# Optimization experiments

Hardware: AMD Instinct MI355X
Metric: run time of the kernel (lower is better)

The kernel has to match this reference:

```python
import jax, jax.numpy as jnp
import numpy as np


def _eta(pos, conj):
    # e[0] = pos[:,1::2] repeated into even/odd cols; e[1] = (+/-)pos[:,0::2] likewise
    c = jnp.repeat(pos[:, 1::2], 2, axis=1)
    s = jnp.repeat(pos[:, 0::2], 2, axis=1)
    return jnp.stack([c, s if conj else -s])  # [2, N, d]


def setup_inputs() -> dict:
    key = jax.random.key(0)
    ks = jax.random.split(key, 8)
    B, N, d, H = 8, 4096, 128, 4
    s = 0.02
    return {
        "x": jax.random.normal(ks[0], (B, N, d), jnp.float32),
        "pos": jax.random.normal(ks[1], (N, d), jnp.float32),
        "W_lt": jax.random.normal(ks[2], (d, d), jnp.float32) * s,
        "W_phi": jax.random.normal(ks[3], (d * H, d), jnp.float32) * s,
        "b_phi": jnp.zeros((d * H,), jnp.float32),
        "W_c1": jax.random.normal(ks[4], (H, H), jnp.float32) * s,
        "b_c1": jnp.zeros((H,), jnp.float32),
        "W_c2": jax.random.normal(ks[5], (1, H), jnp.float32) * s,
        "b_c2": jnp.zeros((1,), jnp.float32),
        "ln_g": jnp.ones((d,), jnp.float32),
        "ln_b": jnp.zeros((d,), jnp.float32),
        "W_f1": jax.random.normal(ks[6], (d, d), jnp.float32) * s,
        "b_f1": jnp.zeros((d,), jnp.float32),
        "W_f2": jax.random.normal(ks[7], (d, d), jnp.float32) * s,
        "b_f2": jnp.zeros((d,), jnp.float32),
    }


def reference(x, pos, W_lt, W_phi, b_phi, W_c1, b_c1, W_c2, b_c2,
              ln_g, ln_b, W_f1, b_f1, W_f2, b_f2):
    B, N, d = x.shape
    H = W_phi.shape[0] // d
    x = x @ W_lt.T                                   # linear_trans (no bias)
    e = _eta(pos, False)                             # [2,N,d]
    xe = x[None] * e[:, None]                        # [2,B,N,d]
    # A = ones(N,N) - I  =>  A @ v == sum over nodes minus self
    f = xe.sum(axis=2, keepdims=True) - xe           # [2,B,N,d]
    f_norm = jnp.sqrt(f[0] ** 2 + f[1] ** 2)         # [B,N,d]
    phi = ((x + pos[None]) @ W_phi.T + b_phi).reshape(B, N, H, d)
    # ReLU1(|f| - phi): relu(min(1, f_norm - phi))
    res = jax.nn.relu(jnp.minimum(1.0, f_norm[:, :, None, :] - phi))  # [B,N,H,d]
    ce = _eta(pos, True)
    fec = f[0] * ce[0][None] - f[1] * ce[1][None]    # [B,N,d]
    rfe = res * fec[:, :, None, :]                   # [B,N,H,d]
    # inverse transform: (1/N) * (M @ A) with A symmetric => sum-minus-self over node dim
    inv = (rfe.sum(axis=1, keepdims=True) - rfe) / N  # [B,N,H,d]
    t = inv.transpose(0, 1, 3, 2)                    # [B,N,d,H]
    comb = (jax.nn.relu(t @ W_c1.T + b_c1) @ W_c2.T + b_c2)[..., 0]  # [B,N,d]
    m = x + comb
    mu = m.mean(-1, keepdims=True)
    var = ((m - mu) ** 2).mean(-1, keepdims=True)
    mn = (m - mu) * jax.lax.rsqrt(var + 1e-6) * ln_g + ln_b
    return jax.nn.relu(mn @ W_f1.T + b_f1) @ W_f2.T + b_f2
```

## Files before the change

kernel.cpp:

```cpp
#include <hip/hip_runtime.h>
#include <hip/hip_bf16.h>


#define DEV __device__ __forceinline__

typedef __attribute__((ext_vector_type(8))) short bf16x8;
typedef __attribute__((ext_vector_type(4))) float f32x4;

constexpr int Bb = 8, Nn = 4096;
constexpr int BN = Bb * Nn;
constexpr int LDP = 136;

union U8 { ushort u[8]; uint4 v; };

static DEV ushort f2bf(float f) {
    __hip_bfloat16 h = __float2bfloat16(f);
    return *reinterpret_cast<unsigned short*>(&h);
}
static DEV float bf2f(ushort u) {
    return __bfloat162float(*reinterpret_cast<const __hip_bfloat16*>(&u));
}

template <int MODE>
__global__ __launch_bounds__(256) void k_mfma_gemm(
    const void* __restrict__ Xv, const float* __restrict__ W,
    const float* __restrict__ bias, const float* __restrict__ pos,
    ushort* __restrict__ outB)
{
    __shared__ __align__(16) ushort xs[64 * LDP];
    __shared__ __align__(16) ushort wsl[128 * LDP];
    const int t = threadIdx.x;
    const int row0 = blockIdx.x * 64;
    const int jt = (MODE == 1) ? blockIdx.y : 0;

    if (MODE == 0) {
        const float* X = (const float*)Xv;
        #pragma unroll
        for (int i = 0; i < 4; ++i) {
            int e = t + i * 256, r = e >> 4, c = (e & 15) * 8;
            const float* p = X + (size_t)(row0 + r) * 128 + c;
            float4 a = *reinterpret_cast<const float4*>(p);
            float4 b = *reinterpret_cast<const float4*>(p + 4);
            U8 u;
            u.u[0] = f2bf(a.x); u.u[1] = f2bf(a.y); u.u[2] = f2bf(a.z); u.u[3] = f2bf(a.w);
            u.u[4] = f2bf(b.x); u.u[5] = f2bf(b.y); u.u[6] = f2bf(b.z); u.u[7] = f2bf(b.w);
            *reinterpret_cast<uint4*>(xs + r * LDP + c) = u.v;
        }
    } else {
        const ushort* X = (const ushort*)Xv;
        #pragma unroll
        for (int i = 0; i < 4; ++i) {
            int e = t + i * 256, r = e >> 4, c = (e & 15) * 8;
            U8 u;
            u.v = *reinterpret_cast<const uint4*>(X + (size_t)(row0 + r) * 128 + c);
            int n = (row0 + r) & (Nn - 1);
            const float* q = pos + (size_t)n * 128 + c;
            float4 pa = *reinterpret_cast<const float4*>(q);
            float4 pb = *reinterpret_cast<const float4*>(q + 4);
            u.u[0] = f2bf(bf2f(u.u[0]) + pa.x);
            u.u[1] = f2bf(bf2f(u.u[1]) + pa.y);
            u.u[2] = f2bf(bf2f(u.u[2]) + pa.z);
            u.u[3] = f2bf(bf2f(u.u[3]) + pa.w);
            u.u[4] = f2bf(bf2f(u.u[4]) + pb.x);
            u.u[5] = f2bf(bf2f(u.u[5]) + pb.y);
            u.u[6] = f2bf(bf2f(u.u[6]) + pb.z);
            u.u[7] = f2bf(bf2f(u.u[7]) + pb.w);
            *reinterpret_cast<uint4*>(xs + r * LDP + c) = u.v;
        }
    }
    {
        const float* Wt = W + (size_t)jt * 128 * 128;
        #pragma unroll
        for (int i = 0; i < 8; ++i) {
            int e = t + i * 256, r = e >> 4, c = (e & 15) * 8;
            const float* p = Wt + (size_t)r * 128 + c;
            float4 a = *reinterpret_cast<const float4*>(p);
            float4 b = *reinterpret_cast<const float4*>(p + 4);
            U8 u;
            u.u[0] = f2bf(a.x); u.u[1] = f2bf(a.y); u.u[2] = f2bf(a.z); u.u[3] = f2bf(a.w);
            u.u[4] = f2bf(b.x); u.u[5] = f2bf(b.y); u.u[6] = f2bf(b.z); u.u[7] = f2bf(b.w);
            *reinterpret_cast<uint4*>(wsl + r * LDP + c) = u.v;
        }
    }
    __syncthreads();

    const int w = t >> 6, l = t & 63;
    const int lr = l & 15;
    const int lk = (l >> 4) * 8;

    f32x4 acc[8];
    #pragma unroll
    for (int cf = 0; cf < 8; ++cf) acc[cf] = f32x4{0.f, 0.f, 0.f, 0.f};

    #pragma unroll
    for (int ks = 0; ks < 4; ++ks) {
        bf16x8 a = *reinterpret_cast<const bf16x8*>(xs + (w * 16 + lr) * LDP + ks * 32 + lk);
        #pragma unroll
        for (int cf = 0; cf < 8; ++cf) {
            bf16x8 b = *reinterpret_cast<const bf16x8*>(wsl + (cf * 16 + lr) * LDP + ks * 32 + lk);
            acc[cf] = __builtin_amdgcn_mfma_f32_16x16x32_bf16(a, b, acc[cf], 0, 0, 0);
        }
    }

    __syncthreads();

    #pragma unroll
    for (int cf = 0; cf < 8; ++cf) {
        int col = cf * 16 + lr;
        float bv = (MODE == 1) ? bias[jt * 128 + col] : 0.f;
        #pragma unroll
        for (int reg = 0; reg < 4; ++reg) {
            int rl = w * 16 + (l >> 4) * 4 + reg;
            xs[rl * LDP + col] = f2bf(acc[cf][reg] + bv);
        }
    }
    __syncthreads();

    #pragma unroll
    for (int i = 0; i < 4; ++i) {
        int e = t + i * 256, r = e >> 4, c = (e & 15) * 8;
        uint4 v = *reinterpret_cast<const uint4*>(xs + r * LDP + c);
        if (MODE == 0)
            *reinterpret_cast<uint4*>(outB + (size_t)(row0 + r) * 128 + c) = v;
        else
            *reinterpret_cast<uint4*>(outB + (size_t)(row0 + r) * 512 + jt * 128 + c) = v;
    }
}

__global__ __launch_bounds__(256) void k_reduceS(
    const ushort* __restrict__ x1b, const float* __restrict__ pos,
    float* __restrict__ PS)
{
    int b = blockIdx.x >> 6, c64 = blockIdx.x & 63;
    int rr = threadIdx.x >> 5, d0 = (threadIdx.x & 31) * 4;
    float a0[4] = {0,0,0,0}, a1[4] = {0,0,0,0};
    #pragma unroll
    for (int i = 0; i < 8; ++i) {
        int n = c64 * 64 + i * 8 + rr;
        size_t r = (size_t)b * Nn + n;
        ushort4 xv = *reinterpret_cast<const ushort4*>(x1b + r * 128 + d0);
        float4 p = *reinterpret_cast<const float4*>(pos + (size_t)n * 128 + d0);
        float x0 = bf2f(xv.x), x1 = bf2f(xv.y), x2 = bf2f(xv.z), x3 = bf2f(xv.w);
        a0[0] += x0 * p.y; a1[0] += x0 * p.x;
        a0[1] += x1 * p.y; a1[1] += x1 * p.x;
        a0[2] += x2 * p.w; a1[2] += x2 * p.z;
        a0[3] += x3 * p.w; a1[3] += x3 * p.z;
    }
    __shared__ float redA[8][128], redB[8][128];
    #pragma unroll
    for (int j = 0; j < 4; ++j) { redA[rr][d0 + j] = a0[j]; redB[rr][d0 + j] = a1[j]; }
    __syncthreads();
    int tt = threadIdx.x;
    float s = 0.f;
    if (tt < 128) {
        #pragma unroll
        for (int k = 0; k < 8; ++k) s += redA[k][tt];
    } else {
        #pragma unroll
        for (int k = 0; k < 8; ++k) s += redB[k][tt - 128];
    }
    PS[(size_t)blockIdx.x * 256 + tt] = s;
}

__global__ __launch_bounds__(256) void k_finS(
    const float* __restrict__ PS, float* __restrict__ S0, float* __restrict__ S1)
{
    int b = blockIdx.x, t = threadIdx.x;
    float s = 0.f;
    #pragma unroll 8
    for (int c = 0; c < 64; ++c) s += PS[(size_t)(b * 64 + c) * 256 + t];
    if (t < 128) S0[b * 128 + t] = s;
    else         S1[b * 128 + (t - 128)] = s;
}

__global__ __launch_bounds__(256) void k_reduceT(
    const ushort* __restrict__ x1b, const ushort* __restrict__ phi,
    const float* __restrict__ pos, const float* __restrict__ S0,
    const float* __restrict__ S1, float* __restrict__ PT)
{
    int b = blockIdx.x >> 6, c64 = blockIdx.x & 63;
    int rr = threadIdx.x >> 5, d0 = (threadIdx.x & 31) * 4;
    float4 S0v = *reinterpret_cast<const float4*>(S0 + b * 128 + d0);
    float4 S1v = *reinterpret_cast<const float4*>(S1 + b * 128 + d0);
    float acc[4][4];
    #pragma unroll
    for (int h = 0; h < 4; ++h)
        #pragma unroll
        for (int j = 0; j < 4; ++j) acc[h][j] = 0.f;

    #pragma unroll 2
    for (int i = 0; i < 8; ++i) {
        int n = c64 * 64 + i * 8 + rr;
        size_t r = (size_t)b * Nn + n;
        ushort4 xv4 = *reinterpret_cast<const ushort4*>(x1b + r * 128 + d0);
        float4 p = *reinterpret_cast<const float4*>(pos + (size_t)n * 128 + d0);
        float xv[4] = {bf2f(xv4.x), bf2f(xv4.y), bf2f(xv4.z), bf2f(xv4.w)};
        float cc[4] = {p.y, p.y, p.w, p.w};
        float ss[4] = {p.x, p.x, p.z, p.z};
        float fec[4], fn[4];
        #pragma unroll
        for (int j = 0; j < 4; ++j) {
            float f0 = ((j < 2) ? ((j == 0) ? S0v.x : S0v.y) : ((j == 2) ? S0v.z : S0v.w)) - xv[j] * cc[j];
            float f1 = xv[j] * ss[j] - ((j < 2) ? ((j == 0) ? S1v.x : S1v.y) : ((j == 2) ? S1v.z : S1v.w));
            fn[j] = sqrtf(f0 * f0 + f1 * f1);
            fec[j] = f0 * cc[j] - f1 * ss[j];
        }
        #pragma unroll
        for (int h = 0; h < 4; ++h) {
            ushort4 ph4 = *reinterpret_cast<const ushort4*>(phi + r * 512 + h * 128 + d0);
            float ph[4] = {bf2f(ph4.x), bf2f(ph4.y), bf2f(ph4.z), bf2f(ph4.w)};
            #pragma unroll
            for (int j = 0; j < 4; ++j)
                acc[h][j] += fmaxf(0.f, fminf(1.f, fn[j] - ph[j])) * fec[j];
        }
    }
    __shared__ float red[8][512];
    #pragma unroll
    for (int h = 0; h < 4; ++h)
        #pragma unroll
        for (int j = 0; j < 4; ++j) red[rr][h * 128 + d0 + j] = acc[h][j];
    __syncthreads();
    int tt = threadIdx.x;
    #pragma unroll
    for (int q = 0; q < 2; ++q) {
        int idx = tt + q * 256;
        float s = 0.f;
        #pragma unroll
        for (int k = 0; k < 8; ++k) s += red[k][idx];
        PT[(size_t)blockIdx.x * 512 + idx] = s;
    }
}

__global__ __launch_bounds__(256) void k_finT(
    const float* __restrict__ PT, float* __restrict__ T)
{
    int idx = blockIdx.x * 256 + threadIdx.x;
    int b = idx >> 9, lo = idx & 511;
    float s = 0.f;
    #pragma unroll 8
    for (int c = 0; c < 64; ++c) s += PT[(size_t)b * 32768 + c * 512 + lo];
    T[idx] = s;
}

__global__ __launch_bounds__(256) void k_comb_ln(
    const ushort* __restrict__ x1b, const ushort* __restrict__ phi,
    const float* __restrict__ pos, const float* __restrict__ S0,
    const float* __restrict__ S1, const float* __restrict__ T,
    const float* __restrict__ Wc1, const float* __restrict__ bc1,
    const float* __restrict__ Wc2, const float* __restrict__ bc2,
    const float* __restrict__ lng, const float* __restrict__ lnb,
    ushort* __restrict__ mnB)
{
    int w = threadIdx.x >> 6, l = threadIdx.x & 63;
    int rrow = blockIdx.x * 4 + w;
    int b = rrow >> 12;
    int n = rrow & 4095;
    int d0 = 2 * l;
    size_t r = (size_t)rrow;

    ushort2 xv2 = *reinterpret_cast<const ushort2*>(x1b + r * 128 + d0);
    float2 p2 = *reinterpret_cast<const float2*>(pos + (size_t)n * 128 + d0);
    float2 s0 = *reinterpret_cast<const float2*>(S0 + b * 128 + d0);
    float2 s1 = *reinterpret_cast<const float2*>(S1 + b * 128 + d0);
    float cc = p2.y, ss = p2.x;

    float m[2];
    float xv[2] = {bf2f(xv2.x), bf2f(xv2.y)};
    float S0a[2] = {s0.x, s0.y}, S1a[2] = {s1.x, s1.y};
    #pragma unroll
    for (int q = 0; q < 2; ++q) {
        float f0 = S0a[q] - xv[q] * cc;
        float f1 = xv[q] * ss - S1a[q];
        float fn = sqrtf(f0 * f0 + f1 * f1);
        float fec = f0 * cc - f1 * ss;
        float inv[4];
        #pragma unroll
        for (int h = 0; h < 4; ++h) {
            float ph = bf2f(phi[r * 512 + h * 128 + d0 + q]);
            float res = fmaxf(0.f, fminf(1.f, fn - ph));
            inv[h] = (T[(b * 4 + h) * 128 + d0 + q] - res * fec) * (1.f / (float)Nn);
        }
        float comb = bc2[0];
        #pragma unroll
        for (int h = 0; h < 4; ++h) {
            float u = bc1[h];
            #pragma unroll
            for (int h2 = 0; h2 < 4; ++h2) u += Wc1[h * 4 + h2] * inv[h2];
            comb += fmaxf(u, 0.f) * Wc2[h];
        }
        m[q] = xv[q] + comb;
    }

    float s = m[0] + m[1];
    #pragma unroll
    for (int off = 32; off; off >>= 1) s += __shfl_xor(s, off);
    float mu = s * (1.f / 128.f);
    float e0 = m[0] - mu, e1 = m[1] - mu;
    float v = e0 * e0 + e1 * e1;
    #pragma unroll
    for (int off = 32; off; off >>= 1) v += __shfl_xor(v, off);
    float rstd = rsqrtf(v * (1.f / 128.f) + 1e-6f);
    ushort2 o;
    o.x = f2bf(e0 * rstd * lng[d0] + lnb[d0]);
    o.y = f2bf(e1 * rstd * lng[d0 + 1] + lnb[d0 + 1]);
    *reinterpret_cast<ushort2*>(mnB + r * 128 + d0) = o;
}

__global__ __launch_bounds__(256) void k_ffn(
    const ushort* __restrict__ mnB, const float* __restrict__ Wf1,
    const float* __restrict__ bf1, const float* __restrict__ Wf2,
    const float* __restrict__ bf2, float* __restrict__ out)
{
    __shared__ __align__(16) ushort xs[64 * LDP];
    __shared__ __align__(16) ushort wsl[128 * LDP];
    const int t = threadIdx.x;
    const int row0 = blockIdx.x * 64;

    #pragma unroll
    for (int i = 0; i < 4; ++i) {
        int e = t + i * 256, r = e >> 4, c = (e & 15) * 8;
        uint4 v = *reinterpret_cast<const uint4*>(mnB + (size_t)(row0 + r) * 128 + c);
        *reinterpret_cast<uint4*>(xs + r * LDP + c) = v;
    }
    #pragma unroll
    for (int i = 0; i < 8; ++i) {
        int e = t + i * 256, r = e >> 4, c = (e & 15) * 8;
        const float* p = Wf1 + (size_t)r * 128 + c;
        float4 a = *reinterpret_cast<const float4*>(p);
        float4 b = *reinterpret_cast<const float4*>(p + 4);
        U8 u;
        u.u[0] = f2bf(a.x); u.u[1] = f2bf(a.y); u.u[2] = f2bf(a.z); u.u[3] = f2bf(a.w);
        u.u[4] = f2bf(b.x); u.u[5] = f2bf(b.y); u.u[6] = f2bf(b.z); u.u[7] = f2bf(b.w);
        *reinterpret_cast<uint4*>(wsl + r * LDP + c) = u.v;
    }
    __syncthreads();

    const int w = t >> 6, l = t & 63;
    const int lr = l & 15;
    const int lk = (l >> 4) * 8;

    f32x4 acc[8];
    #pragma unroll
    for (int cf = 0; cf < 8; ++cf) acc[cf] = f32x4{0.f, 0.f, 0.f, 0.f};
    #pragma unroll
    for (int ks = 0; ks < 4; ++ks) {
        bf16x8 a = *reinterpret_cast<const bf16x8*>(xs + (w * 16 + lr) * LDP + ks * 32 + lk);
        #pragma unroll
        for (int cf = 0; cf < 8; ++cf) {
            bf16x8 b = *reinterpret_cast<const bf16x8*>(wsl + (cf * 16 + lr) * LDP + ks * 32 + lk);
            acc[cf] = __builtin_amdgcn_mfma_f32_16x16x32_bf16(a, b, acc[cf], 0, 0, 0);
        }
    }

    __syncthreads();

    #pragma unroll
    for (int cf = 0; cf < 8; ++cf) {
        int col = cf * 16 + lr;
        float bv = bf1[col];
        #pragma unroll
        for (int reg = 0; reg < 4; ++reg) {
            int rl = w * 16 + (l >> 4) * 4 + reg;
            xs[rl * LDP + col] = f2bf(fmaxf(acc[cf][reg] + bv, 0.f));
        }
    }
    #pragma unroll
    for (int i = 0; i < 8; ++i) {
        int e = t + i * 256, r = e >> 4, c = (e & 15) * 8;
        const float* p = Wf2 + (size_t)r * 128 + c;
        float4 a = *reinterpret_cast<const float4*>(p);
        float4 b = *reinterpret_cast<const float4*>(p + 4);
        U8 u;
        u.u[0] = f2bf(a.x); u.u[1] = f2bf(a.y); u.u[2] = f2bf(a.z); u.u[3] = f2bf(a.w);
        u.u[4] = f2bf(b.x); u.u[5] = f2bf(b.y); u.u[6] = f2bf(b.z); u.u[7] = f2bf(b.w);
        *reinterpret_cast<uint4*>(wsl + r * LDP + c) = u.v;
    }
    __syncthreads();

    #pragma unroll
    for (int cf = 0; cf < 8; ++cf) acc[cf] = f32x4{0.f, 0.f, 0.f, 0.f};
    #pragma unroll
    for (int ks = 0; ks < 4; ++ks) {
        bf16x8 a = *reinterpret_cast<const bf16x8*>(xs + (w * 16 + lr) * LDP + ks * 32 + lk);
        #pragma unroll
        for (int cf = 0; cf < 8; ++cf) {
            bf16x8 b = *reinterpret_cast<const bf16x8*>(wsl + (cf * 16 + lr) * LDP + ks * 32 + lk);
            acc[cf] = __builtin_amdgcn_mfma_f32_16x16x32_bf16(a, b, acc[cf], 0, 0, 0);
        }
    }

    #pragma unroll
    for (int cf = 0; cf < 8; ++cf) {
        int col = cf * 16 + lr;
        float bv = bf2[col];
        #pragma unroll
        for (int reg = 0; reg < 4; ++reg) {
            int r = row0 + w * 16 + (l >> 4) * 4 + reg;
            out[(size_t)r * 128 + col] = acc[cf][reg] + bv;
        }
    }
}

extern "C" void kernel_launch(void* const* d_in, const int* in_sizes, int n_in,
                              void* d_out, int out_size, void* d_ws, size_t ws_size,
                              hipStream_t stream)
{
    const float* x    = (const float*)d_in[0];
    const float* pos  = (const float*)d_in[1];
    const float* Wlt  = (const float*)d_in[2];
    const float* Wphi = (const float*)d_in[3];
    const float* bphi = (const float*)d_in[4];
    const float* Wc1  = (const float*)d_in[5];
    const float* bc1  = (const float*)d_in[6];
    const float* Wc2  = (const float*)d_in[7];
    const float* bc2  = (const float*)d_in[8];
    const float* lng  = (const float*)d_in[9];
    const float* lnb  = (const float*)d_in[10];
    const float* Wf1  = (const float*)d_in[11];
    const float* bf1  = (const float*)d_in[12];
    const float* Wf2  = (const float*)d_in[13];
    const float* bf2  = (const float*)d_in[14];

    float* ws = (float*)d_ws;
    ushort* x1b = (ushort*)ws;
    ushort* mnB = (ushort*)(ws + 2097152);
    float* S0   = ws + 4194304;
    float* S1   = S0 + 1024;
    float* T    = S1 + 1024;
    float* PS   = T + 4096;
    float* PT   = PS + 131072;
    ushort* phi = (ushort*)(ws + 4593664);
    float* out  = (float*)d_out;

    k_mfma_gemm<0><<<dim3(BN / 64), 256, 0, stream>>>(x, Wlt, nullptr, pos, x1b);
    k_reduceS<<<dim3(512), 256, 0, stream>>>(x1b, pos, PS);
    k_finS<<<dim3(Bb), 256, 0, stream>>>(PS, S0, S1);
    k_mfma_gemm<1><<<dim3(BN / 64, 4), 256, 0, stream>>>(x1b, Wphi, bphi, pos, phi);
    k_reduceT<<<dim3(512), 256, 0, stream>>>(x1b, phi, pos, S0, S1, PT);
    k_finT<<<dim3(16), 256, 0, stream>>>(PT, T);
    k_comb_ln<<<dim3(BN / 4), 256, 0, stream>>>(x1b, phi, pos, S0, S1, T,
                                                Wc1, bc1, Wc2, bc2, lng, lnb, mnB);
    k_ffn<<<dim3(BN / 64), 256, 0, stream>>>(mnB, Wf1, bf1, Wf2, bf2, out);
}
```

Baseline: 71.44 us.

## Store phi in FP8 and fuse combine/LayerNorm into the FFN kernel

The phi projection output is now written as FP8 e4m3 instead of bf16, halving the bytes that the reduction and combine stages read. The separate combine+LayerNorm kernel is folded into the FFN kernel: each block computes its 64 normalized rows directly into shared memory, which removes the intermediate bf16 buffer round-trip and one launch. The FP8 quantization of phi lowers precision in the threshold term and may affect accuracy.

```diff
diff --git a/kernel.cpp b/kernel.cpp
--- a/kernel.cpp
+++ b/kernel.cpp
@@ -1,5 +1,6 @@
 #include <hip/hip_runtime.h>
 #include <hip/hip_bf16.h>
+#include <hip/hip_fp8.h>
 
 
 #define DEV __device__ __forceinline__
@@ -10,6 +11,7 @@
 constexpr int Bb = 8, Nn = 4096;
 constexpr int BN = Bb * Nn;
 constexpr int LDP = 136;
+constexpr int P8  = 144;
 
 union U8 { ushort u[8]; uint4 v; };
 
@@ -19,13 +21,22 @@
 }
 static DEV float bf2f(ushort u) {
     return __bfloat162float(*reinterpret_cast<const __hip_bfloat16*>(&u));
+}
+static DEV unsigned char f2fp8(float f) {
+    __hip_fp8_e4m3 q(f);
+    return q.__x;
+}
+static DEV float fp82f(unsigned char u) {
+    __hip_fp8_e4m3 q;
+    q.__x = u;
+    return (float)q;
 }
 
 template <int MODE>
 __global__ __launch_bounds__(256) void k_mfma_gemm(
     const void* __restrict__ Xv, const float* __restrict__ W,
     const float* __restrict__ bias, const float* __restrict__ pos,
-    ushort* __restrict__ outB)
+    ushort* __restrict__ outB, unsigned char* __restrict__ out8)
 {
     __shared__ __align__(16) ushort xs[64 * LDP];
     __shared__ __align__(16) ushort wsl[128 * LDP];
@@ -104,26 +115,42 @@
 
     __syncthreads();
 
-    #pragma unroll
-    for (int cf = 0; cf < 8; ++cf) {
-        int col = cf * 16 + lr;
-        float bv = (MODE == 1) ? bias[jt * 128 + col] : 0.f;
-        #pragma unroll
-        for (int reg = 0; reg < 4; ++reg) {
-            int rl = w * 16 + (l >> 4) * 4 + reg;
-            xs[rl * LDP + col] = f2bf(acc[cf][reg] + bv);
-        }
-    }
-    __syncthreads();
-
-    #pragma unroll
-    for (int i = 0; i < 4; ++i) {
-        int e = t + i * 256, r = e >> 4, c = (e & 15) * 8;
-        uint4 v = *reinterpret_cast<const uint4*>(xs + r * LDP + c);
-        if (MODE == 0)
+    if (MODE == 0) {
+        #pragma unroll
+        for (int cf = 0; cf < 8; ++cf) {
+            int col = cf * 16 + lr;
+            #pragma unroll
+            for (int reg = 0; reg < 4; ++reg) {
+                int rl = w * 16 + (l >> 4) * 4 + reg;
+                xs[rl * LDP + col] = f2bf(acc[cf][reg]);
+            }
+        }
+        __syncthreads();
+        #pragma unroll
+        for (int i = 0; i < 4; ++i) {
+            int e = t + i * 256, r = e >> 4, c = (e & 15) * 8;
+            uint4 v = *reinterpret_cast<const uint4*>(xs + r * LDP + c);
             *reinterpret_cast<uint4*>(outB + (size_t)(row0 + r) * 128 + c) = v;
-        else
-            *reinterpret_cast<uint4*>(outB + (size_t)(row0 + r) * 512 + jt * 128 + c) = v;
+        }
+    } else {
+        unsigned char* x8 = reinterpret_cast<unsigned char*>(xs);
+        #pragma unroll
+        for (int cf = 0; cf < 8; ++cf) {
+            int col = cf * 16 + lr;
+            float bv = bias[jt * 128 + col];
+            #pragma unroll
+            for (int reg = 0; reg < 4; ++reg) {
+                int rl = w * 16 + (l >> 4) * 4 + reg;
+                x8[rl * P8 + col] = f2fp8(acc[cf][reg] + bv);
+            }
+        }
+        __syncthreads();
+        #pragma unroll
+        for (int i = 0; i < 2; ++i) {
+            int e = t + i * 256, r = e >> 3, c = (e & 7) * 16;
+            uint4 v = *reinterpret_cast<const uint4*>(x8 + r * P8 + c);
+            *reinterpret_cast<uint4*>(out8 + (size_t)(row0 + r) * 512 + jt * 128 + c) = v;
+        }
     }
 }
 
@@ -174,7 +201,7 @@
 }
 
 __global__ __launch_bounds__(256) void k_reduceT(
-    const ushort* __restrict__ x1b, const ushort* __restrict__ phi,
+    const ushort* __restrict__ x1b, const unsigned char* __restrict__ phi8,
     const float* __restrict__ pos, const float* __restrict__ S0,
     const float* __restrict__ S1, float* __restrict__ PT)
 {
@@ -182,6 +209,8 @@
     int rr = threadIdx.x >> 5, d0 = (threadIdx.x & 31) * 4;
     float4 S0v = *reinterpret_cast<const float4*>(S0 + b * 128 + d0);
     float4 S1v = *reinterpret_cast<const float4*>(S1 + b * 128 + d0);
+    float S0a[4] = {S0v.x, S0v.y, S0v.z, S0v.w};
+    float S1a[4] = {S1v.x, S1v.y, S1v.z, S1v.w};
     float acc[4][4];
     #pragma unroll
     for (int h = 0; h < 4; ++h)
@@ -200,15 +229,15 @@
         float fec[4], fn[4];
         #pragma unroll
         for (int j = 0; j < 4; ++j) {
-            float f0 = ((j < 2) ? ((j == 0) ? S0v.x : S0v.y) : ((j == 2) ? S0v.z : S0v.w)) - xv[j] * cc[j];
-            float f1 = xv[j] * ss[j] - ((j < 2) ? ((j == 0) ? S1v.x : S1v.y) : ((j == 2) ? S1v.z : S1v.w));
+            float f0 = S0a[j] - xv[j] * cc[j];
+            float f1 = xv[j] * ss[j] - S1a[j];
             fn[j] = sqrtf(f0 * f0 + f1 * f1);
             fec[j] = f0 * cc[j] - f1 * ss[j];
         }
         #pragma unroll
         for (int h = 0; h < 4; ++h) {
-            ushort4 ph4 = *reinterpret_cast<const ushort4*>(phi + r * 512 + h * 128 + d0);
-            float ph[4] = {bf2f(ph4.x), bf2f(ph4.y), bf2f(ph4.z), bf2f(ph4.w)};
+            uchar4 ph4 = *reinterpret_cast<const uchar4*>(phi8 + r * 512 + h * 128 + d0);
+            float ph[4] = {fp82f(ph4.x), fp82f(ph4.y), fp82f(ph4.z), fp82f(ph4.w)};
             #pragma unroll
             for (int j = 0; j < 4; ++j)
                 acc[h][j] += fmaxf(0.f, fminf(1.f, fn[j] - ph[j])) * fec[j];
@@ -242,86 +271,23 @@
     T[idx] = s;
 }
 
-__global__ __launch_bounds__(256) void k_comb_ln(
-    const ushort* __restrict__ x1b, const ushort* __restrict__ phi,
+__global__ __launch_bounds__(256) void k_comb_ffn(
+    const ushort* __restrict__ x1b, const unsigned char* __restrict__ phi8,
     const float* __restrict__ pos, const float* __restrict__ S0,
     const float* __restrict__ S1, const float* __restrict__ T,
     const float* __restrict__ Wc1, const float* __restrict__ bc1,
     const float* __restrict__ Wc2, const float* __restrict__ bc2,
     const float* __restrict__ lng, const float* __restrict__ lnb,
-    ushort* __restrict__ mnB)
-{
-    int w = threadIdx.x >> 6, l = threadIdx.x & 63;
-    int rrow = blockIdx.x * 4 + w;
-    int b = rrow >> 12;
-    int n = rrow & 4095;
-    int d0 = 2 * l;
-    size_t r = (size_t)rrow;
-
-    ushort2 xv2 = *reinterpret_cast<const ushort2*>(x1b + r * 128 + d0);
-    float2 p2 = *reinterpret_cast<const float2*>(pos + (size_t)n * 128 + d0);
-    float2 s0 = *reinterpret_cast<const float2*>(S0 + b * 128 + d0);
-    float2 s1 = *reinterpret_cast<const float2*>(S1 + b * 128 + d0);
-    float cc = p2.y, ss = p2.x;
-
-    float m[2];
-    float xv[2] = {bf2f(xv2.x), bf2f(xv2.y)};
-    float S0a[2] = {s0.x, s0.y}, S1a[2] = {s1.x, s1.y};
-    #pragma unroll
-    for (int q = 0; q < 2; ++q) {
-        float f0 = S0a[q] - xv[q] * cc;
-        float f1 = xv[q] * ss - S1a[q];
-        float fn = sqrtf(f0 * f0 + f1 * f1);
-        float fec = f0 * cc - f1 * ss;
-        float inv[4];
-        #pragma unroll
-        for (int h = 0; h < 4; ++h) {
-            float ph = bf2f(phi[r * 512 + h * 128 + d0 + q]);
-            float res = fmaxf(0.f, fminf(1.f, fn - ph));
-            inv[h] = (T[(b * 4 + h) * 128 + d0 + q] - res * fec) * (1.f / (float)Nn);
-        }
-        float comb = bc2[0];
-        #pragma unroll
-        for (int h = 0; h < 4; ++h) {
-            float u = bc1[h];
-            #pragma unroll
-            for (int h2 = 0; h2 < 4; ++h2) u += Wc1[h * 4 + h2] * inv[h2];
-            comb += fmaxf(u, 0.f) * Wc2[h];
-        }
-        m[q] = xv[q] + comb;
-    }
-
-    float s = m[0] + m[1];
-    #pragma unroll
-    for (int off = 32; off; off >>= 1) s += __shfl_xor(s, off);
-    float mu = s * (1.f / 128.f);
-    float e0 = m[0] - mu, e1 = m[1] - mu;
-    float v = e0 * e0 + e1 * e1;
-    #pragma unroll
-    for (int off = 32; off; off >>= 1) v += __shfl_xor(v, off);
-    float rstd = rsqrtf(v * (1.f / 128.f) + 1e-6f);
-    ushort2 o;
-    o.x = f2bf(e0 * rstd * lng[d0] + lnb[d0]);
-    o.y = f2bf(e1 * rstd * lng[d0 + 1] + lnb[d0 + 1]);
-    *reinterpret_cast<ushort2*>(mnB + r * 128 + d0) = o;
-}
-
-__global__ __launch_bounds__(256) void k_ffn(
-    const ushort* __restrict__ mnB, const float* __restrict__ Wf1,
-    const float* __restrict__ bf1, const float* __restrict__ Wf2,
-    const float* __restrict__ bf2, float* __restrict__ out)
+    const float* __restrict__ Wf1, const float* __restrict__ bf1,
+    const float* __restrict__ Wf2, const float* __restrict__ bf2,
+    float* __restrict__ out)
 {
     __shared__ __align__(16) ushort xs[64 * LDP];
     __shared__ __align__(16) ushort wsl[128 * LDP];
     const int t = threadIdx.x;
     const int row0 = blockIdx.x * 64;
-
-    #pragma unroll
-    for (int i = 0; i < 4; ++i) {
-        int e = t + i * 256, r = e >> 4, c = (e & 15) * 8;
-        uint4 v = *reinterpret_cast<const uint4*>(mnB + (size_t)(row0 + r) * 128 + c);
-        *reinterpret_cast<uint4*>(xs + r * LDP + c) = v;
-    }
+    const int w = t >> 6, l = t & 63;
+
     #pragma unroll
     for (int i = 0; i < 8; ++i) {
         int e = t + i * 256, r = e >> 4, c = (e & 15) * 8;
@@ -333,9 +299,80 @@
         u.u[4] = f2bf(b.x); u.u[5] = f2bf(b.y); u.u[6] = f2bf(b.z); u.u[7] = f2bf(b.w);
         *reinterpret_cast<uint4*>(wsl + r * LDP + c) = u.v;
     }
-    __syncthreads();
-
-    const int w = t >> 6, l = t & 63;
+
+    {
+        const int d0 = 2 * l;
+        const float g0 = lng[d0], g1 = lng[d0 + 1];
+        const float be0 = lnb[d0], be1 = lnb[d0 + 1];
+        const float c20 = Wc2[0], c21 = Wc2[1], c22 = Wc2[2], c23 = Wc2[3];
+        const float b2v = bc2[0];
+        for (int i = 0; i < 16; ++i) {
+            int rl = w * 16 + i;
+            int rrow = row0 + rl;
+            int b = rrow >> 12;
+            int n = rrow & 4095;
+            size_t r = (size_t)rrow;
+
+            ushort2 xv2 = *reinterpret_cast<const ushort2*>(x1b + r * 128 + d0);
+            float2 p2 = *reinterpret_cast<const float2*>(pos + (size_t)n * 128 + d0);
+            float2 s0 = *reinterpret_cast<const float2*>(S0 + b * 128 + d0);
+            float2 s1 = *reinterpret_cast<const float2*>(S1 + b * 128 + d0);
+            float cc = p2.y, ss = p2.x;
+            float xv[2] = {bf2f(xv2.x), bf2f(xv2.y)};
+            float S0a[2] = {s0.x, s0.y}, S1a[2] = {s1.x, s1.y};
+            float2 Tv[4];
+            #pragma unroll
+            for (int h = 0; h < 4; ++h)
+                Tv[h] = *reinterpret_cast<const float2*>(T + (b * 4 + h) * 128 + d0);
+            uchar2 ph2[4];
+            #pragma unroll
+            for (int h = 0; h < 4; ++h)
+                ph2[h] = *reinterpret_cast<const uchar2*>(phi8 + r * 512 + h * 128 + d0);
+
+            float m[2];
+            #pragma unroll
+            for (int q = 0; q < 2; ++q) {
+                float f0 = S0a[q] - xv[q] * cc;
+                float f1 = xv[q] * ss - S1a[q];
+                float fn = sqrtf(f0 * f0 + f1 * f1);
+                float fec = f0 * cc - f1 * ss;
+                float inv[4];
+                #pragma unroll
+                for (int h = 0; h < 4; ++h) {
+                    float ph = fp82f(q ? ph2[h].y : ph2[h].x);
+                    float res = fmaxf(0.f, fminf(1.f, fn - ph));
+                    float tv = q ? Tv[h].y : Tv[h].x;
+                    inv[h] = (tv - res * fec) * (1.f / (float)Nn);
+                }
+                float comb = b2v;
+                float wc2a[4] = {c20, c21, c22, c23};
+                #pragma unroll
+                for (int h = 0; h < 4; ++h) {
+                    float u = bc1[h];
+                    #pragma unroll
+                    for (int h2 = 0; h2 < 4; ++h2) u += Wc1[h * 4 + h2] * inv[h2];
+                    comb += fmaxf(u, 0.f) * wc2a[h];
+                }
+                m[q] = xv[q] + comb;
+            }
+
+            float s = m[0] + m[1];
+            #pragma unroll
+            for (int off = 32; off; off >>= 1) s += __shfl_xor(s, off);
+            float mu = s * (1.f / 128.f);
+            float e0 = m[0] - mu, e1 = m[1] - mu;
+            float v = e0 * e0 + e1 * e1;
+            #pragma unroll
+            for (int off = 32; off; off >>= 1) v += __shfl_xor(v, off);
+            float rstd = rsqrtf(v * (1.f / 128.f) + 1e-6f);
+            ushort2 o;
+            o.x = f2bf(e0 * rstd * g0 + be0);
+            o.y = f2bf(e1 * rstd * g1 + be1);
+            *reinterpret_cast<ushort2*>(xs + rl * LDP + d0) = o;
+        }
+    }
+    __syncthreads();
+
     const int lr = l & 15;
     const int lk = (l >> 4) * 8;
 
@@ -351,7 +388,6 @@
             acc[cf] = __builtin_amdgcn_mfma_f32_16x16x32_bf16(a, b, acc[cf], 0, 0, 0);
         }
     }
-
     __syncthreads();
 
     #pragma unroll
@@ -388,7 +424,6 @@
             acc[cf] = __builtin_amdgcn_mfma_f32_16x16x32_bf16(a, b, acc[cf], 0, 0, 0);
         }
     }
-
     #pragma unroll
     for (int cf = 0; cf < 8; ++cf) {
         int col = cf * 16 + lr;
@@ -423,22 +458,21 @@
 
     float* ws = (float*)d_ws;
     ushort* x1b = (ushort*)ws;
-    ushort* mnB = (ushort*)(ws + 2097152);
-    float* S0   = ws + 4194304;
+    float* S0   = ws + 2097152;
     float* S1   = S0 + 1024;
     float* T    = S1 + 1024;
     float* PS   = T + 4096;
     float* PT   = PS + 131072;
-    ushort* phi = (ushort*)(ws + 4593664);
+    unsigned char* phi8 = (unsigned char*)(ws + 2496512);
     float* out  = (float*)d_out;
 
-    k_mfma_gemm<0><<<dim3(BN / 64), 256, 0, stream>>>(x, Wlt, nullptr, pos, x1b);
+    k_mfma_gemm<0><<<dim3(BN / 64), 256, 0, stream>>>(x, Wlt, nullptr, pos, x1b, nullptr);
     k_reduceS<<<dim3(512), 256, 0, stream>>>(x1b, pos, PS);
     k_finS<<<dim3(Bb), 256, 0, stream>>>(PS, S0, S1);
-    k_mfma_gemm<1><<<dim3(BN / 64, 4), 256, 0, stream>>>(x1b, Wphi, bphi, pos, phi);
-    k_reduceT<<<dim3(512), 256, 0, stream>>>(x1b, phi, pos, S0, S1, PT);
+    k_mfma_gemm<1><<<dim3(BN / 64, 4), 256, 0, stream>>>(x1b, Wphi, bphi, pos, nullptr, phi8);
+    k_reduceT<<<dim3(512), 256, 0, stream>>>(x1b, phi8, pos, S0, S1, PT);
     k_finT<<<dim3(16), 256, 0, stream>>>(PT, T);
-    k_comb_ln<<<dim3(BN / 4), 256, 0, stream>>>(x1b, phi, pos, S0, S1, T,
-                                                Wc1, bc1, Wc2, bc2, lng, lnb, mnB);
-    k_ffn<<<dim3(BN / 64), 256, 0, stream>>>(mnB, Wf1, bf1, Wf2, bf2, out);
-}
+    k_comb_ffn<<<dim3(BN / 64), 256, 0, stream>>>(x1b, phi8, pos, S0, S1, T,
+                                                  Wc1, bc1, Wc2, bc2, lng, lnb,
+                                                  Wf1, bf1, Wf2, bf2, out);
+}
```

Result: slower. 73.61 us (+3.0%).
